# Kernel tuning notes

Measured on AMD Instinct MI355X. Metric: run time of the kernel, lower is better.

The kernel has to match this reference:

```python
import jax, jax.numpy as jnp
import numpy as np

B, T, HID = 2, 2048, 2048
NH, NKV, D = 16, 4, 128
WIN = 512
ROPE_BASE = 10000.0
SCALE = D ** -0.5
EPS = 1e-12


def setup_inputs() -> dict:
    key = jax.random.key(0)
    ks = jax.random.split(key, 5)
    x = jax.random.normal(ks[0], (B, T, HID), dtype=jnp.float32)
    wq = jax.random.normal(ks[1], (HID, NH * D), dtype=jnp.float32) * 0.02
    wk = jax.random.normal(ks[2], (HID, NKV * D), dtype=jnp.float32) * 0.02
    wv = jax.random.normal(ks[3], (HID, NKV * D), dtype=jnp.float32) * 0.02
    wo = jax.random.normal(ks[4], (NH * D, HID), dtype=jnp.float32) * 0.02
    return {"x": x, "wq": wq, "wk": wk, "wv": wv, "wo": wo}


def _rope_tables(t, offset=0):
    inv_freq = 1.0 / (ROPE_BASE ** (jnp.arange(0, D, 2, dtype=jnp.float32) / D))
    pos = jnp.arange(offset, offset + t, dtype=jnp.float32)
    freqs = pos[:, None] * inv_freq[None, :]              # [t, D/2]
    cos = jnp.concatenate([jnp.cos(freqs), jnp.cos(freqs)], axis=-1)  # [t, D]
    sin = jnp.concatenate([jnp.sin(freqs), jnp.sin(freqs)], axis=-1)
    return cos, sin


def _apply_rope(x, cos, sin):
    # x: [B, H, T, D]; rotate-half formulation
    x1, x2 = jnp.split(x, 2, axis=-1)
    rot = jnp.concatenate([-x2, x1], axis=-1)
    return x * cos[None, None] + rot * sin[None, None]


def _l2norm(x):
    n = jnp.sqrt(jnp.sum(x * x, axis=-1, keepdims=True))
    return x / jnp.maximum(n, EPS)


def _forward(x, wq, wk, wv, wo):
    b, t, _ = x.shape
    q = (x @ wq).reshape(b, t, NH, D).transpose(0, 2, 1, 3)    # [B,H,T,D]
    k = (x @ wk).reshape(b, t, NKV, D).transpose(0, 2, 1, 3)   # [B,Hk,T,D]
    v = (x @ wv).reshape(b, t, NKV, D).transpose(0, 2, 1, 3)
    q = _l2norm(q)
    k = _l2norm(k)
    cos, sin = _rope_tables(t, offset=0)
    q = _apply_rope(q, cos, sin)
    k = _apply_rope(k, cos, sin)
    rep = NH // NKV
    k = jnp.repeat(k, rep, axis=1)                             # GQA repeat_interleave
    v = jnp.repeat(v, rep, axis=1)
    i = jnp.arange(t)
    allowed = (i[None, :] <= i[:, None]) & (i[None, :] > i[:, None] - WIN)  # [T,T]
    logits = jnp.einsum("bhid,bhjd->bhij", q, k) * SCALE
    logits = jnp.where(allowed[None, None], logits, -jnp.inf)
    attn = jax.nn.softmax(logits, axis=-1)
    out = jnp.einsum("bhij,bhjd->bhid", attn, v)
    out = out.transpose(0, 2, 1, 3).reshape(b, t, NH * D)
    return out @ wo


def reference(x, wq, wk, wv, wo):
    return _forward(x, wq, wk, wv, wo)
```

## Files before the change

kernel.cpp:

```cpp
#include <hip/hip_runtime.h>
#include <hip/hip_bf16.h>
#include <cstdint>

#define NHQ 16
#define NKVH 4
#define HDIM 128
#define WINSZ 512
#define TSEQ 2048
#define ATTN_SCALE 0.08838834764831845f

typedef __attribute__((ext_vector_type(8))) short s16x8;
typedef __attribute__((ext_vector_type(4))) float f32x4;

__device__ __forceinline__ void gload16(const void* g, void* lds) {
  __builtin_amdgcn_global_load_lds(
      (const __attribute__((address_space(1))) unsigned int*)g,
      (__attribute__((address_space(3))) unsigned int*)(uintptr_t)lds,
      16, 0, 0);
}

__device__ __forceinline__ f32x4 mfma16(s16x8 a, s16x8 b, f32x4 c) {
  return __builtin_amdgcn_mfma_f32_16x16x32_bf16(a, b, c, 0, 0, 0);
}

#define SBAR() asm volatile("s_barrier" ::: "memory")
#define VMCNT(n) asm volatile("s_waitcnt vmcnt(" #n ")" ::: "memory")
#define LGKM(n) asm volatile("s_waitcnt lgkmcnt(" #n ")" ::: "memory")

__global__ __launch_bounds__(256) void rope_tables_kernel(float* __restrict__ cosT,
                                                          float* __restrict__ sinT) {
  int idx = blockIdx.x * 256 + threadIdx.x;
  int t = idx >> 6, d2 = idx & 63;
  float inv = powf(10000.0f, -(float)d2 / 64.0f);
  float a = (float)t * inv;
  cosT[idx] = cosf(a);
  sinT[idx] = sinf(a);
}

__global__ __launch_bounds__(256) void cast_kernel(const float* __restrict__ in,
                                                   __bf16* __restrict__ out, int n4) {
  int i = blockIdx.x * 256 + threadIdx.x;
  if (i >= n4) return;
  float4 v = ((const float4*)in)[i];
  union { __bf16 h[4]; uint2 u; } pk;
  pk.h[0] = (__bf16)v.x; pk.h[1] = (__bf16)v.y; pk.h[2] = (__bf16)v.z; pk.h[3] = (__bf16)v.w;
  ((uint2*)out)[i] = pk.u;
}

__global__ __launch_bounds__(256) void transpose_cast(const float* __restrict__ in,
                                                      __bf16* __restrict__ out, int R, int C) {
  __shared__ float tile[32][33];
  int c0 = blockIdx.x * 32, r0 = blockIdx.y * 32;
  int tx = threadIdx.x, ty = threadIdx.y;
#pragma unroll
  for (int i = 0; i < 4; i++)
    tile[ty + i * 8][tx] = in[(size_t)(r0 + ty + i * 8) * C + c0 + tx];
  __syncthreads();
#pragma unroll
  for (int i = 0; i < 4; i++)
    out[(size_t)(c0 + ty + i * 8) * R + r0 + tx] = (__bf16)tile[tx][ty + i * 8];
}

template <int MODE>
__global__ __launch_bounds__(512, 2) void gemm8(const __bf16* __restrict__ A,
                                                const __bf16* __restrict__ Bt,
                                                float* __restrict__ Cf,
                                                __bf16* __restrict__ Qo, __bf16* __restrict__ Ko,
                                                __bf16* __restrict__ Vo, int M, int N, int K) {
  __shared__ __attribute__((aligned(16))) char Lds[2][65536];

  const int tid = threadIdx.x;
  const int w = tid >> 6, lane = tid & 63;
  const int wm = w >> 2, wn = w & 3;

  const int nbx = gridDim.x;
  const int nwg = nbx * gridDim.y;
  const int bid = blockIdx.y * nbx + blockIdx.x;
  const int q8 = nwg >> 3, r8 = nwg & 7;
  const int xcd = bid & 7, idx = bid >> 3;
  const int swz = (xcd < r8 ? xcd * (q8 + 1) : r8 * (q8 + 1) + (xcd - r8) * q8) + idx;
  const int bx = swz % nbx, by = swz / nbx;
  const int m0 = by * 256, n0 = bx * 256;

  const int ru = tid >> 3;
  const int cs = (tid & 7) ^ (ru & 7);
  const __bf16* gAs = A + (size_t)(m0 + ru) * K + cs * 8;
  const __bf16* gBs = Bt + (size_t)(n0 + ru) * K + cs * 8;

  auto stA = [&](int tt, int u) {
    gload16(gAs + (size_t)(64 * u) * K + tt * 64, Lds[tt & 1] + u * 8192 + w * 1024);
  };
  auto stB = [&](int tt, int u) {
    gload16(gBs + (size_t)(64 * u) * K + tt * 64, Lds[tt & 1] + 32768 + u * 8192 + w * 1024);
  };

  const int rowb = (lane & 15) * 128;
  const int cph0 = (((lane >> 4)) ^ (lane & 7)) * 16;
  const int cph1 = ((4 + (lane >> 4)) ^ (lane & 7)) * 16;
  const int Abase = wm * 16384;
  const int Bbase = 32768 + wn * 8192;

  f32x4 acc[8][4];
  f32x4 zero = {0.f, 0.f, 0.f, 0.f};
#pragma unroll
  for (int i = 0; i < 8; i++)
#pragma unroll
    for (int j = 0; j < 4; j++) acc[i][j] = zero;

  const int NT = K >> 6;

#pragma unroll
  for (int u = 0; u < 4; u++) stA(0, u);
#pragma unroll
  for (int u = 0; u < 4; u++) stB(0, u);
#pragma unroll
  for (int u = 0; u < 4; u++) stA(1, u);
#pragma unroll
  for (int u = 0; u < 4; u++) stB(1, u);
  VMCNT(8);
  SBAR();

  s16x8 fa[4][2], fb[4][2];

  for (int t = 0; t < NT; ++t) {
    const char* bs = Lds[t & 1];
    const bool more = (t + 2) < NT;

#pragma unroll
    for (int mi = 0; mi < 4; mi++) {
      fa[mi][0] = *(const s16x8*)(bs + Abase + mi * 2048 + rowb + cph0);
      fa[mi][1] = *(const s16x8*)(bs + Abase + mi * 2048 + rowb + cph1);
    }
#pragma unroll
    for (int ni = 0; ni < 2; ni++) {
      fb[ni][0] = *(const s16x8*)(bs + Bbase + ni * 2048 + rowb + cph0);
      fb[ni][1] = *(const s16x8*)(bs + Bbase + ni * 2048 + rowb + cph1);
    }
    SBAR();
    LGKM(0);
    __builtin_amdgcn_sched_barrier(0);
    __builtin_amdgcn_s_setprio(1);
#pragma unroll
    for (int mi = 0; mi < 4; mi++)
#pragma unroll
      for (int ni = 0; ni < 2; ni++)
#pragma unroll
        for (int kk = 0; kk < 2; kk++)
          acc[mi][ni] = mfma16(fa[mi][kk], fb[ni][kk], acc[mi][ni]);
    __builtin_amdgcn_s_setprio(0);
    SBAR();

#pragma unroll
    for (int ni = 2; ni < 4; ni++) {
      fb[ni][0] = *(const s16x8*)(bs + Bbase + ni * 2048 + rowb + cph0);
      fb[ni][1] = *(const s16x8*)(bs + Bbase + ni * 2048 + rowb + cph1);
    }
    if (more) { stA(t + 2, 0); stA(t + 2, 2); }
    SBAR();
    LGKM(0);
    __builtin_amdgcn_sched_barrier(0);
    __builtin_amdgcn_s_setprio(1);
#pragma unroll
    for (int mi = 0; mi < 4; mi++)
#pragma unroll
      for (int ni = 2; ni < 4; ni++)
#pragma unroll
        for (int kk = 0; kk < 2; kk++)
          acc[mi][ni] = mfma16(fa[mi][kk], fb[ni][kk], acc[mi][ni]);
    __builtin_amdgcn_s_setprio(0);
    SBAR();

#pragma unroll
    for (int mi = 0; mi < 4; mi++) {
      fa[mi][0] = *(const s16x8*)(bs + Abase + 8192 + mi * 2048 + rowb + cph0);
      fa[mi][1] = *(const s16x8*)(bs + Abase + 8192 + mi * 2048 + rowb + cph1);
    }
    if (more) { stB(t + 2, 0); stB(t + 2, 1); stB(t + 2, 2); stB(t + 2, 3); }
    SBAR();
    LGKM(0);
    __builtin_amdgcn_sched_barrier(0);
    __builtin_amdgcn_s_setprio(1);
#pragma unroll
    for (int mi = 0; mi < 4; mi++)
#pragma unroll
      for (int ni = 0; ni < 2; ni++)
#pragma unroll
        for (int kk = 0; kk < 2; kk++)
          acc[4 + mi][ni] = mfma16(fa[mi][kk], fb[ni][kk], acc[4 + mi][ni]);
    __builtin_amdgcn_s_setprio(0);
    SBAR();

    if (more) { stA(t + 2, 1); stA(t + 2, 3); }
    if (t + 2 < NT) {
      VMCNT(8);
    } else if (t + 1 < NT) {
      VMCNT(0);
    }
    SBAR();
    __builtin_amdgcn_s_setprio(1);
#pragma unroll
    for (int mi = 0; mi < 4; mi++)
#pragma unroll
      for (int ni = 2; ni < 4; ni++)
#pragma unroll
        for (int kk = 0; kk < 2; kk++)
          acc[4 + mi][ni] = mfma16(fa[mi][kk], fb[ni][kk], acc[4 + mi][ni]);
    __builtin_amdgcn_s_setprio(0);
    SBAR();
  }

#pragma unroll
  for (int mf = 0; mf < 8; mf++)
#pragma unroll
    for (int nf = 0; nf < 4; nf++) {
      int rbase = m0 + wm * 128 + mf * 16 + (lane >> 4) * 4;
      int col = n0 + wn * 64 + nf * 16 + (lane & 15);
#pragma unroll
      for (int r = 0; r < 4; r++) {
        int m = rbase + r;
        float v = acc[mf][nf][r];
        if constexpr (MODE == 0) {
          Cf[(size_t)m * N + col] = v;
        } else {
          int b = m >> 11, tq = m & 2047;
          __bf16 bv = (__bf16)v;
          if (col < 2048) {
            Qo[(((size_t)(b * NHQ + (col >> 7))) * TSEQ + tq) * HDIM + (col & 127)] = bv;
          } else if (col < 2560) {
            int c2 = col - 2048;
            Ko[(((size_t)(b * NKVH + (c2 >> 7))) * TSEQ + tq) * HDIM + (c2 & 127)] = bv;
          } else {
            int c2 = col - 2560;
            Vo[(((size_t)(b * NKVH + (c2 >> 7))) * TSEQ + tq) * HDIM + (c2 & 127)] = bv;
          }
        }
      }
    }
}

__global__ __launch_bounds__(256) void normrope(__bf16* __restrict__ Q, __bf16* __restrict__ Kk,
                                                const float* __restrict__ cosT,
                                                const float* __restrict__ sinT) {
  int w = threadIdx.x >> 6, lane = threadIdx.x & 63;
  int row = blockIdx.x / 5;
  int slot = (blockIdx.x % 5) * 4 + w;
  int b = row >> 11, t = row & 2047;
  __bf16* p;
  if (slot < 16)
    p = Q + (((size_t)(b * NHQ + slot)) * TSEQ + t) * HDIM;
  else
    p = Kk + (((size_t)(b * NKVH + (slot - 16))) * TSEQ + t) * HDIM;
  float x1 = (float)p[lane], x2 = (float)p[lane + 64];
  float ss = x1 * x1 + x2 * x2;
#pragma unroll
  for (int off = 32; off; off >>= 1) ss += __shfl_xor(ss, off);
  float inv = 1.0f / fmaxf(sqrtf(ss), 1e-12f);
  x1 *= inv;
  x2 *= inv;
  float c = cosT[t * 64 + lane], s = sinT[t * 64 + lane];
  p[lane] = (__bf16)(x1 * c - x2 * s);
  p[lane + 64] = (__bf16)(x2 * c + x1 * s);
}

__global__ __launch_bounds__(256) void attn_kernel(const __bf16* __restrict__ Qf,
                                                   const __bf16* __restrict__ Kf,
                                                   const __bf16* __restrict__ Vf,
                                                   __bf16* __restrict__ Ab) {
  __shared__ __attribute__((aligned(16))) char KlB[64 * 256];
  __shared__ __attribute__((aligned(16))) char VtB[128 * 128];
  __shared__ __attribute__((aligned(16))) char PlB[4 * 2048];
  int tid = threadIdx.x, w = tid >> 6, lane = tid & 63;
  int bid = blockIdx.x;
  int qt = bid & 31, h = (bid >> 5) & 15, b = bid >> 9;
  int qs = qt * 64;
  int kvh = h >> 2;
  const __bf16* Qb = Qf + ((size_t)(b * NHQ + h) * TSEQ) * HDIM;
  const __bf16* Kb = Kf + ((size_t)(b * NKVH + kvh) * TSEQ) * HDIM;
  const __bf16* Vb = Vf + ((size_t)(b * NKVH + kvh) * TSEQ) * HDIM;
  char* Pw = PlB + w * 2048;

  s16x8 aq[4];
  int qrow_f = qs + w * 16 + (lane & 15);
#pragma unroll
  for (int kb = 0; kb < 4; kb++)
    aq[kb] = *(const s16x8*)(Qb + (size_t)qrow_f * HDIM + kb * 32 + (lane >> 4) * 8);

  f32x4 acc[8];
  f32x4 zero = {0.f, 0.f, 0.f, 0.f};
#pragma unroll
  for (int db = 0; db < 8; db++) acc[db] = zero;
  float mrow[4], lrow[4];
#pragma unroll
  for (int r = 0; r < 4; r++) { mrow[r] = -1e30f; lrow[r] = 0.f; }

  int lo = qs - (WINSZ - 1);
  if (lo < 0) lo = 0;
  lo &= ~63;
  const int nt = ((qs + 64) - lo) >> 6;

  const int kjr = tid >> 4, kkc = tid & 15;
  const int vk = tid & 63, vg = tid >> 6;

  int4 kA[4], vA[4], kB[4], vB[4];

#define ATTN_LOAD(KR, VR, KS)                                                      \
  _Pragma("unroll") for (int i = 0; i < 4; i++) {                                  \
    KR[i] = *(const int4*)(Kb + (size_t)((KS) + kjr + 16 * i) * HDIM + kkc * 8);   \
    VR[i] = *(const int4*)(Vb + (size_t)((KS) + vk) * HDIM + (vg + 4 * i) * 8);    \
  }

#define ATTN_WRITE(KR, VR)                                                         \
  _Pragma("unroll") for (int i = 0; i < 4; i++) {                                  \
    int jr = kjr + 16 * i;                                                         \
    *(int4*)(KlB + jr * 256 + ((kkc * 16) ^ ((jr & 7) << 4))) = KR[i];             \
    const __bf16* pv = (const __bf16*)&VR[i];                                      \
    int d0 = (vg + 4 * i) * 8;                                                     \
    _Pragma("unroll") for (int e = 0; e < 8; e++) {                                \
      int d = d0 + e;                                                              \
      *(__bf16*)(VtB + d * 128 + ((vk * 2) ^ ((d & 7) << 4))) = pv[e];             \
    }                                                                              \
  }

#define ATTN_COMPUTE(KS)                                                           \
  {                                                                                \
    f32x4 sacc[4];                                                                 \
    _Pragma("unroll") for (int jb = 0; jb < 4; jb++) sacc[jb] = zero;              \
    _Pragma("unroll") for (int jb = 0; jb < 4; jb++) {                             \
      int key = jb * 16 + (lane & 15);                                             \
      _Pragma("unroll") for (int kb = 0; kb < 4; kb++) {                           \
        s16x8 bk = *(const s16x8*)(KlB + key * 256 +                               \
                                   ((kb * 64 + (lane >> 4) * 16) ^ ((key & 7) << 4))); \
        sacc[jb] = mfma16(aq[kb], bk, sacc[jb]);                                   \
      }                                                                            \
    }                                                                              \
    float scf[4];                                                                  \
    _Pragma("unroll") for (int r = 0; r < 4; r++) {                                \
      int qrow = qs + w * 16 + (lane >> 4) * 4 + r;                                \
      float sv[4]; bool av[4];                                                     \
      _Pragma("unroll") for (int jb = 0; jb < 4; jb++) {                           \
        int j = (KS) + jb * 16 + (lane & 15);                                      \
        av[jb] = (j <= qrow) && (j > qrow - WINSZ);                                \
        sv[jb] = sacc[jb][r] * ATTN_SCALE;                                         \
      }                                                                            \
      float mt = -1e30f;                                                           \
      _Pragma("unroll") for (int jb = 0; jb < 4; jb++)                             \
        mt = fmaxf(mt, av[jb] ? sv[jb] : -1e30f);                                  \
      _Pragma("unroll") for (int off = 1; off < 16; off <<= 1)                     \
        mt = fmaxf(mt, __shfl_xor(mt, off));                                       \
      float mn = fmaxf(mrow[r], mt);                                               \
      float pv_[4]; float ts = 0.f;                                                \
      _Pragma("unroll") for (int jb = 0; jb < 4; jb++) {                           \
        pv_[jb] = av[jb] ? __expf(sv[jb] - mn) : 0.f;                              \
        ts += pv_[jb];                                                             \
      }                                                                            \
      _Pragma("unroll") for (int off = 1; off < 16; off <<= 1)                     \
        ts += __shfl_xor(ts, off);                                                 \
      float sf = __expf(mrow[r] - mn);                                             \
      lrow[r] = lrow[r] * sf + ts;                                                 \
      mrow[r] = mn;                                                                \
      scf[r] = sf;                                                                 \
      int q = (lane >> 4) * 4 + r;                                                 \
      _Pragma("unroll") for (int jb = 0; jb < 4; jb++)                             \
        *(__bf16*)(Pw + q * 128 +                                                  \
                   (((jb * 16 + (lane & 15)) * 2) ^ ((q & 7) << 4))) = (__bf16)pv_[jb]; \
    }                                                                              \
    s16x8 pa[2];                                                                   \
    _Pragma("unroll") for (int kb = 0; kb < 2; kb++) {                             \
      int q = lane & 15;                                                           \
      pa[kb] = *(const s16x8*)(Pw + q * 128 +                                      \
                               ((kb * 64 + (lane >> 4) * 16) ^ ((q & 7) << 4)));   \
    }                                                                              \
    _Pragma("unroll") for (int db = 0; db < 8; db++) {                             \
      f32x4 tt = acc[db];                                                          \
      _Pragma("unroll") for (int r = 0; r < 4; r++) tt[r] *= scf[r];               \
      acc[db] = tt;                                                                \
    }                                                                              \
    _Pragma("unroll") for (int db = 0; db < 8; db++) {                             \
      int d = db * 16 + (lane & 15);                                               \
      _Pragma("unroll") for (int kb = 0; kb < 2; kb++) {                           \
        s16x8 bv = *(const s16x8*)(VtB + d * 128 +                                 \
                                   ((kb * 64 + (lane >> 4) * 16) ^ ((d & 7) << 4))); \
        acc[db] = mfma16(pa[kb], bv, acc[db]);                                     \
      }                                                                            \
    }                                                                              \
  }

  int ks = lo;
  ATTN_LOAD(kA, vA, lo);
  for (int t = 0; t < nt; ++t) {
    if ((t & 1) == 0) {
      ATTN_WRITE(kA, vA);
      if (t + 1 < nt) ATTN_LOAD(kB, vB, ks + 64);
    } else {
      ATTN_WRITE(kB, vB);
      if (t + 1 < nt) ATTN_LOAD(kA, vA, ks + 64);
    }
    __syncthreads();
    ATTN_COMPUTE(ks);
    __syncthreads();
    ks += 64;
  }

#undef ATTN_LOAD
#undef ATTN_WRITE
#undef ATTN_COMPUTE

#pragma unroll
  for (int db = 0; db < 8; db++)
#pragma unroll
    for (int r = 0; r < 4; r++) {
      int qrow = qs + w * 16 + (lane >> 4) * 4 + r;
      float v = acc[db][r] / lrow[r];
      Ab[((size_t)(b * TSEQ + qrow)) * 2048 + h * HDIM + db * 16 + (lane & 15)] = (__bf16)v;
    }
}

extern "C" void kernel_launch(void* const* d_in, const int* in_sizes, int n_in,
                              void* d_out, int out_size, void* d_ws, size_t ws_size,
                              hipStream_t stream) {
  const float* x = (const float*)d_in[0];
  const float* wq = (const float*)d_in[1];
  const float* wk = (const float*)d_in[2];
  const float* wv = (const float*)d_in[3];
  const float* wo = (const float*)d_in[4];
  float* out = (float*)d_out;

  char* ws = (char*)d_ws;
  size_t off = 0;
  auto alloc = [&](size_t bytes) -> void* {
    void* p = ws + off;
    off += (bytes + 255) & ~(size_t)255;
    return p;
  };
  __bf16* Xb = (__bf16*)alloc((size_t)4096 * 2048 * 2);
  __bf16* Wqkvt = (__bf16*)alloc((size_t)3072 * 2048 * 2);
  __bf16* Wot = (__bf16*)alloc((size_t)2048 * 2048 * 2);
  __bf16* Q = (__bf16*)alloc((size_t)2 * NHQ * TSEQ * HDIM * 2);
  __bf16* Kb = (__bf16*)alloc((size_t)2 * NKVH * TSEQ * HDIM * 2);
  __bf16* Vb = (__bf16*)alloc((size_t)2 * NKVH * TSEQ * HDIM * 2);
  float* cosT = (float*)alloc((size_t)TSEQ * 64 * 4);
  float* sinT = (float*)alloc((size_t)TSEQ * 64 * 4);
  __bf16* Ab = Xb;

  rope_tables_kernel<<<TSEQ * 64 / 256, 256, 0, stream>>>(cosT, sinT);
  cast_kernel<<<8192, 256, 0, stream>>>(x, Xb, 2097152);
  dim3 tb(32, 8);
  transpose_cast<<<dim3(64, 64), tb, 0, stream>>>(wq, Wqkvt, 2048, 2048);
  transpose_cast<<<dim3(16, 64), tb, 0, stream>>>(wk, Wqkvt + (size_t)2048 * 2048, 2048, 512);
  transpose_cast<<<dim3(16, 64), tb, 0, stream>>>(wv, Wqkvt + (size_t)2560 * 2048, 2048, 512);
  transpose_cast<<<dim3(64, 64), tb, 0, stream>>>(wo, Wot, 2048, 2048);

  gemm8<1><<<dim3(12, 16), 512, 0, stream>>>(Xb, Wqkvt, nullptr, Q, Kb, Vb, 4096, 3072, 2048);
  normrope<<<4096 * 5, 256, 0, stream>>>(Q, Kb, cosT, sinT);
  attn_kernel<<<2 * NHQ * (TSEQ / 64), 256, 0, stream>>>(Q, Kb, Vb, Ab);
  gemm8<0><<<dim3(8, 16), 512, 0, stream>>>(Ab, Wot, out, nullptr, nullptr, nullptr, 4096, 2048,
                                            2048);
}
```

Measured before the change: 242.7 us.

## Enlarge attention query tile to 128 rows with 8 waves and skip masked tiles

The attention kernel now uses 512 threads per block covering 128 query rows, so each K/V tile staged in shared memory is shared by twice as many waves. Waves whose 16 query rows fall wholly outside a key tile's causal window skip that tile's compute. The double-buffered register prefetch becomes a single register stage written to LDS after a barrier, and s_setprio raises wave priority around the MFMA loops. In exchange there are half as many blocks, more barriers per tile, and less load/compute overlap.

```diff
diff --git a/kernel.cpp b/kernel.cpp
--- a/kernel.cpp
+++ b/kernel.cpp
@@ -262,17 +262,18 @@
   p[lane + 64] = (__bf16)(x2 * c + x1 * s);
 }
 
-__global__ __launch_bounds__(256) void attn_kernel(const __bf16* __restrict__ Qf,
-                                                   const __bf16* __restrict__ Kf,
-                                                   const __bf16* __restrict__ Vf,
-                                                   __bf16* __restrict__ Ab) {
+__global__ __launch_bounds__(512, 4) void attn_kernel(const __bf16* __restrict__ Qf,
+                                                      const __bf16* __restrict__ Kf,
+                                                      const __bf16* __restrict__ Vf,
+                                                      __bf16* __restrict__ Ab) {
   __shared__ __attribute__((aligned(16))) char KlB[64 * 256];
   __shared__ __attribute__((aligned(16))) char VtB[128 * 128];
-  __shared__ __attribute__((aligned(16))) char PlB[4 * 2048];
+  __shared__ __attribute__((aligned(16))) char PlB[8 * 2048];
   int tid = threadIdx.x, w = tid >> 6, lane = tid & 63;
   int bid = blockIdx.x;
-  int qt = bid & 31, h = (bid >> 5) & 15, b = bid >> 9;
-  int qs = qt * 64;
+  int qt = bid & 15, bh = bid >> 4;
+  int b = bh >> 4, h = bh & 15;
+  int qs = qt * 128;
   int kvh = h >> 2;
   const __bf16* Qb = Qf + ((size_t)(b * NHQ + h) * TSEQ) * HDIM;
   const __bf16* Kb = Kf + ((size_t)(b * NKVH + kvh) * TSEQ) * HDIM;
@@ -296,25 +297,24 @@
   int lo = qs - (WINSZ - 1);
   if (lo < 0) lo = 0;
   lo &= ~63;
-  const int nt = ((qs + 64) - lo) >> 6;
-
-  const int kjr = tid >> 4, kkc = tid & 15;
+  const int nt = ((qs + 128) - lo) >> 6;
+
+  const int kjr = tid >> 3, kkc = tid & 7;
   const int vk = tid & 63, vg = tid >> 6;
 
-  int4 kA[4], vA[4], kB[4], vB[4];
-
-#define ATTN_LOAD(KR, VR, KS)                                                      \
-  _Pragma("unroll") for (int i = 0; i < 4; i++) {                                  \
-    KR[i] = *(const int4*)(Kb + (size_t)((KS) + kjr + 16 * i) * HDIM + kkc * 8);   \
-    VR[i] = *(const int4*)(Vb + (size_t)((KS) + vk) * HDIM + (vg + 4 * i) * 8);    \
+  int4 kR[2], vR[2];
+
+#define ATTN_LOAD(KS)                                                              \
+  _Pragma("unroll") for (int i = 0; i < 2; i++) {                                  \
+    kR[i] = *(const int4*)(Kb + (size_t)((KS) + kjr) * HDIM + (kkc + 8 * i) * 8);  \
+    vR[i] = *(const int4*)(Vb + (size_t)((KS) + vk) * HDIM + (vg + 8 * i) * 8);    \
   }
 
-#define ATTN_WRITE(KR, VR)                                                         \
-  _Pragma("unroll") for (int i = 0; i < 4; i++) {                                  \
-    int jr = kjr + 16 * i;                                                         \
-    *(int4*)(KlB + jr * 256 + ((kkc * 16) ^ ((jr & 7) << 4))) = KR[i];             \
-    const __bf16* pv = (const __bf16*)&VR[i];                                      \
-    int d0 = (vg + 4 * i) * 8;                                                     \
+#define ATTN_WRITE()                                                               \
+  _Pragma("unroll") for (int i = 0; i < 2; i++) {                                  \
+    *(int4*)(KlB + kjr * 256 + (((kkc + 8 * i) * 16) ^ ((kjr & 7) << 4))) = kR[i]; \
+    const __bf16* pv = (const __bf16*)&vR[i];                                      \
+    int d0 = (vg + 8 * i) * 8;                                                     \
     _Pragma("unroll") for (int e = 0; e < 8; e++) {                                \
       int d = d0 + e;                                                              \
       *(__bf16*)(VtB + d * 128 + ((vk * 2) ^ ((d & 7) << 4))) = pv[e];             \
@@ -325,6 +325,7 @@
   {                                                                                \
     f32x4 sacc[4];                                                                 \
     _Pragma("unroll") for (int jb = 0; jb < 4; jb++) sacc[jb] = zero;              \
+    __builtin_amdgcn_s_setprio(1);                                                 \
     _Pragma("unroll") for (int jb = 0; jb < 4; jb++) {                             \
       int key = jb * 16 + (lane & 15);                                             \
       _Pragma("unroll") for (int kb = 0; kb < 4; kb++) {                           \
@@ -333,6 +334,7 @@
         sacc[jb] = mfma16(aq[kb], bk, sacc[jb]);                                   \
       }                                                                            \
     }                                                                              \
+    __builtin_amdgcn_s_setprio(0);                                                 \
     float scf[4];                                                                  \
     _Pragma("unroll") for (int r = 0; r < 4; r++) {                                \
       int qrow = qs + w * 16 + (lane >> 4) * 4 + r;                                \
@@ -375,6 +377,7 @@
       _Pragma("unroll") for (int r = 0; r < 4; r++) tt[r] *= scf[r];               \
       acc[db] = tt;                                                                \
     }                                                                              \
+    __builtin_amdgcn_s_setprio(1);                                                 \
     _Pragma("unroll") for (int db = 0; db < 8; db++) {                             \
       int d = db * 16 + (lane & 15);                                               \
       _Pragma("unroll") for (int kb = 0; kb < 2; kb++) {                           \
@@ -383,21 +386,23 @@
         acc[db] = mfma16(pa[kb], bv, acc[db]);                                     \
       }                                                                            \
     }                                                                              \
+    __builtin_amdgcn_s_setprio(0);                                                 \
   }
 
+  ATTN_LOAD(lo);
+  ATTN_WRITE();
+  __syncthreads();
+
   int ks = lo;
-  ATTN_LOAD(kA, vA, lo);
   for (int t = 0; t < nt; ++t) {
-    if ((t & 1) == 0) {
-      ATTN_WRITE(kA, vA);
-      if (t + 1 < nt) ATTN_LOAD(kB, vB, ks + 64);
-    } else {
-      ATTN_WRITE(kB, vB);
-      if (t + 1 < nt) ATTN_LOAD(kA, vA, ks + 64);
-    }
+    if (t + 1 < nt) ATTN_LOAD(ks + 64);
+    int qmin = qs + w * 16, qmax = qmin + 15;
+    if (ks <= qmax && ks + 63 > qmin - WINSZ) ATTN_COMPUTE(ks);
     __syncthreads();
-    ATTN_COMPUTE(ks);
-    __syncthreads();
+    if (t + 1 < nt) {
+      ATTN_WRITE();
+      __syncthreads();
+    }
     ks += 64;
   }
 
@@ -452,7 +457,7 @@
 
   gemm8<1><<<dim3(12, 16), 512, 0, stream>>>(Xb, Wqkvt, nullptr, Q, Kb, Vb, 4096, 3072, 2048);
   normrope<<<4096 * 5, 256, 0, stream>>>(Q, Kb, cosT, sinT);
-  attn_kernel<<<2 * NHQ * (TSEQ / 64), 256, 0, stream>>>(Q, Kb, Vb, Ab);
+  attn_kernel<<<2 * NHQ * (TSEQ / 128), 512, 0, stream>>>(Q, Kb, Vb, Ab);
   gemm8<0><<<dim3(8, 16), 512, 0, stream>>>(Ab, Wot, out, nullptr, nullptr, nullptr, 4096, 2048,
                                             2048);
 }
```

Measured after the change: 263.0 us. +8.4%, slower.
